# Kernel tuning notes

Hardware: AMD Instinct MI355X
Metric: run time of the kernel (lower is better)

Reference implementation:

```python
import jax, jax.numpy as jnp
import numpy as np

B, C, H, W = 16, 256, 32, 32
LN_EPS = 1e-5


def setup_inputs() -> dict:
    key = jax.random.key(0)
    ks = jax.random.split(key, 12)
    s = 1.0 / np.sqrt(C)
    x = jax.random.normal(ks[0], (B, C, H, W), dtype=jnp.float32)
    # Linear weights stored as [in, out] (torch stores [out, in]; math is x @ W_in_out + b)
    wq = jax.random.uniform(ks[1], (C, C), jnp.float32, -s, s)
    bq = jax.random.uniform(ks[2], (C,), jnp.float32, -s, s)
    wk = jax.random.uniform(ks[3], (C, C), jnp.float32, -s, s)
    bk = jax.random.uniform(ks[4], (C,), jnp.float32, -s, s)
    wv = jax.random.uniform(ks[5], (C, C), jnp.float32, -s, s)
    bv = jax.random.uniform(ks[6], (C,), jnp.float32, -s, s)
    w1 = jax.random.uniform(ks[7], (C, C), jnp.float32, -s, s)
    b1 = jax.random.uniform(ks[8], (C,), jnp.float32, -s, s)
    w2 = jax.random.uniform(ks[9], (C, C), jnp.float32, -s, s)
    b2 = jax.random.uniform(ks[10], (C,), jnp.float32, -s, s)
    gamma = jnp.ones((C,), jnp.float32)
    beta = jnp.zeros((C,), jnp.float32)
    return {"x": x, "wq": wq, "bq": bq, "wk": wk, "bk": bk, "wv": wv, "bv": bv,
            "w1": w1, "b1": b1, "w2": w2, "b2": b2, "gamma": gamma, "beta": beta}


def reference(x, wq, bq, wk, bk, wv, bv, w1, b1, w2, b2, gamma, beta):
    Bd, Cd, Hd, Wd = x.shape
    t = x.reshape(Bd, Cd, Hd * Wd).transpose(0, 2, 1)  # [B, N, C]
    q = t @ wq + bq
    k = t @ wk + bk
    v = t @ wv + bv
    # matrix[b,i,j] = q[b,i,:] . k[b,j,:]  (no 1/sqrt(d) scaling, as in source)
    m = jnp.einsum('bic,bjc->bij', q, k)
    # softmax over dim=-2 (the query axis i)
    m = jax.nn.softmax(m, axis=-2)
    # att[b,j,c] = sum_i v[b,i,c] * m[b,i,j]  (v^T @ m, then permute)
    att = jnp.einsum('bic,bij->bjc', v, m)  # [B, N, C]
    # MLP (SiLU, hidden = C), dropout p=0 -> identity; DropPath eval -> identity
    att = jax.nn.silu(att @ w1 + b1) @ w2 + b2
    # LayerNorm over channel dim
    mu = jnp.mean(att, axis=-1, keepdims=True)
    var = jnp.var(att, axis=-1, keepdims=True)
    att = (att - mu) * jax.lax.rsqrt(var + LN_EPS) * gamma + beta
    return att.transpose(0, 2, 1).reshape(Bd, Cd, Hd, Wd)
```

## Files before the change

### kernel.cpp

```cpp
#include <hip/hip_runtime.h>

#define BB 16
#define CC 256
#define NN 1024

typedef _Float16 f16;
typedef __attribute__((ext_vector_type(8))) _Float16 half8;
typedef __attribute__((ext_vector_type(4))) float f32x4;

__device__ __forceinline__ half8 ldg8(const f16* p) {
  return *reinterpret_cast<const half8*>(p);
}

__device__ __forceinline__ void gll16(const f16* g, f16* l) {
  __builtin_amdgcn_global_load_lds((const __attribute__((address_space(1))) void*)g,
                                   (__attribute__((address_space(3))) void*)l, 16, 0, 0);
}

#define VMCNT(n) asm volatile("s_waitcnt vmcnt(" #n ")" ::: "memory")
#define BAR() __builtin_amdgcn_s_barrier()

__device__ __forceinline__ void stage64k(const f16* __restrict__ g, f16* l, int wave, int lane) {
#pragma unroll
  for (int k = 0; k < 16; ++k) {
    int ob = k * 2048 + wave * 512;
    gll16(g + ob + lane * 8, l + ob);
  }
}

struct WP5 {
  const float* s[5];
  f16* d[5];
};

__global__ void __launch_bounds__(256) k_packW(WP5 p) {
  __shared__ float ws[256][17];
  int m = blockIdx.y, ct = blockIdx.x;
  const float* W = p.s[m];
  f16* wp = p.d[m];
  int tid = threadIdx.x;
  int col = tid & 15, cig = tid >> 4;
#pragma unroll
  for (int pg = 0; pg < 16; ++pg) {
    int ci = pg * 16 + cig;
    ws[ci][col] = W[(size_t)ci * 256 + ct * 16 + col];
  }
  __syncthreads();
  int lane = tid & 63, wave = tid >> 6;
  int row16 = lane & 15, quad = lane >> 4;
#pragma unroll
  for (int kk = 0; kk < 2; ++kk) {
    int kc = wave * 2 + kk;
    half8 o;
#pragma unroll
    for (int j = 0; j < 8; ++j) o[j] = (f16)ws[kc * 32 + quad * 8 + j][row16];
    *reinterpret_cast<half8*>(wp + ((size_t)ct * 8 + kc) * 512 + lane * 8) = o;
  }
}

struct QkvSmem {
  union {
    struct { f16 hi[32][264]; f16 lo[32][264]; } ts;
    f16 ex[2][16][264];
    f16 exv[256][40];
  };
};

__global__ void __launch_bounds__(256) k_qkv(const float* __restrict__ x,
    const f16* __restrict__ wqp, const f16* __restrict__ wkp, const f16* __restrict__ wvp,
    const float* __restrict__ bq, const float* __restrict__ bk, const float* __restrict__ bv,
    f16* __restrict__ qp, f16* __restrict__ kp, f16* __restrict__ vp, int b_base) {
  __shared__ QkvSmem sm;
  int z = blockIdx.z;
  const f16* WT     = (z == 0) ? wqp : (z == 1) ? wkp : wvp;
  const float* bias = (z == 0) ? bq  : (z == 1) ? bk  : bv;
  int bl = blockIdx.x, bg = b_base + bl, n0 = blockIdx.y * 32;
  int tid = threadIdx.x, wave = tid >> 6, lane = tid & 63;
  int row16 = lane & 15, quad = lane >> 4;
  int g = wave >> 1, h = wave & 1;

#pragma unroll
  for (int e = tid; e < 2048; e += 256) {
    int c = e >> 3, n4 = (e & 7) << 2;
    float4 u = *reinterpret_cast<const float4*>(x + (size_t)(bg * CC + c) * NN + n0 + n4);
    float uv[4] = {u.x, u.y, u.z, u.w};
#pragma unroll
    for (int i = 0; i < 4; ++i) {
      f16 hh = (f16)uv[i];
      sm.ts.hi[n4 + i][c] = hh;
      sm.ts.lo[n4 + i][c] = (f16)(uv[i] - (float)hh);
    }
  }
  __syncthreads();

  half8 ah[8], al[8];
#pragma unroll
  for (int kc = 0; kc < 8; ++kc) {
    ah[kc] = *reinterpret_cast<const half8*>(&sm.ts.hi[g * 16 + row16][kc * 32 + quad * 8]);
    al[kc] = *reinterpret_cast<const half8*>(&sm.ts.lo[g * 16 + row16][kc * 32 + quad * 8]);
  }
  __syncthreads();

  if (z < 2) {
    f16* outp = z ? kp : qp;
#pragma unroll
    for (int ct8 = 0; ct8 < 8; ++ct8) {
      int ct = h * 8 + ct8;
      f32x4 acc = {0.f, 0.f, 0.f, 0.f};
      const f16* bh = WT + ((size_t)ct * 8) * 512 + lane * 8;
#pragma unroll
      for (int kc = 0; kc < 8; ++kc) {
        half8 b = ldg8(bh + kc * 512);
        acc = __builtin_amdgcn_mfma_f32_16x16x32_f16(ah[kc], b, acc, 0, 0, 0);
        acc = __builtin_amdgcn_mfma_f32_16x16x32_f16(al[kc], b, acc, 0, 0, 0);
      }
      int co = ct * 16 + row16;
      float bb = bias[co];
#pragma unroll
      for (int r = 0; r < 4; ++r)
        sm.ex[g][quad * 4 + r][co] = (f16)(acc[r] + bb);
    }
    const f16* exr = &sm.ex[g][row16][0];
    size_t fb = ((size_t)bl * 64 + (n0 >> 4) + g) * 8;
#pragma unroll
    for (int k = 0; k < 4; ++k) {
      int kc = h * 4 + k;
      half8 hv = *reinterpret_cast<const half8*>(exr + kc * 32 + quad * 8);
      *reinterpret_cast<half8*>(outp + (fb + kc) * 512 + lane * 8) = hv;
    }
  } else {
#pragma unroll
    for (int ct8 = 0; ct8 < 8; ++ct8) {
      int ct = h * 8 + ct8;
      f32x4 acc = {0.f, 0.f, 0.f, 0.f};
      const f16* bh = WT + ((size_t)ct * 8) * 512 + lane * 8;
#pragma unroll
      for (int kc = 0; kc < 8; ++kc) {
        half8 b = ldg8(bh + kc * 512);
        acc = __builtin_amdgcn_mfma_f32_16x16x32_f16(ah[kc], b, acc, 0, 0, 0);
        acc = __builtin_amdgcn_mfma_f32_16x16x32_f16(al[kc], b, acc, 0, 0, 0);
      }
      int co = ct * 16 + row16;
      float bb = bias[co];
#pragma unroll
      for (int r = 0; r < 4; ++r)
        sm.exv[co][g * 16 + quad * 4 + r] = (f16)(acc[r] + bb);
    }
    __syncthreads();
    size_t vb = ((size_t)bl * 32 + blockIdx.y) * 16;
#pragma unroll
    for (int f = 0; f < 4; ++f) {
      int ct = wave * 4 + f;
      half8 o = *reinterpret_cast<const half8*>(&sm.exv[ct * 16 + row16][quad * 8]);
      *reinterpret_cast<half8*>(vp + (vb + ct) * 512 + lane * 8) = o;
    }
  }
}

struct AttnSmem {
  union {
    struct {
      f16 QB[128 * 256];
      f16 VB[128 * 256];
    } s;
    f16 ex[4][16][264];
  } u;
  f16 P[4][4][16][40];
};

__global__ void __launch_bounds__(256) k_attn_mlp(
    const f16* __restrict__ qp, const f16* __restrict__ kp, const f16* __restrict__ vp,
    const f16* __restrict__ w1p, const float* __restrict__ b1,
    const f16* __restrict__ w2p, const float* __restrict__ b2,
    const float* __restrict__ gamma, const float* __restrict__ beta,
    float* __restrict__ out, int b_base) {
  __shared__ AttnSmem sm;
  int bl = blockIdx.x, bg = b_base + bl;
  int j0 = blockIdx.y * 64;
  int tid = threadIdx.x, wave = tid >> 6, lane = tid & 63;
  int row16 = lane & 15, quad = lane >> 4;
  int jw = j0 + wave * 16;

  const f16* kbase = kp + (size_t)bl * NN * CC;
  int jt = (j0 >> 4) + wave;
  half8 kf[8];
#pragma unroll
  for (int kc = 0; kc < 8; ++kc)
    kf[kc] = ldg8(kbase + ((size_t)jt * 8 + kc) * 512 + lane * 8);

  const f16* qbase = qp + (size_t)bl * NN * CC;
  const f16* vbase = vp + (size_t)bl * CC * NN;

  stage64k(qbase, sm.u.s.QB, wave, lane);
  stage64k(vbase, sm.u.s.VB, wave, lane);
  VMCNT(16);
  BAR();

  f32x4 O[16];
#pragma unroll
  for (int ct = 0; ct < 16; ++ct) O[ct] = {0.f, 0.f, 0.f, 0.f};
  float m_run[4], l_lane[4];
#pragma unroll
  for (int r = 0; r < 4; ++r) { m_run[r] = -1e30f; l_lane[r] = 0.f; }

  for (int it = 0; it < 8; ++it) {
    f32x4 s[8];
#pragma unroll
    for (int f = 0; f < 8; ++f) s[f] = {0.f, 0.f, 0.f, 0.f};
#pragma unroll
    for (int kc = 0; kc < 8; ++kc) {
#pragma unroll
      for (int f = 0; f < 8; ++f) {
        half8 b = *reinterpret_cast<const half8*>(&sm.u.s.QB[(f * 8 + kc) * 512 + lane * 8]);
        s[f] = __builtin_amdgcn_mfma_f32_16x16x32_f16(kf[kc], b, s[f], 0, 0, 0);
      }
    }
    BAR();
    stage64k(qbase + (size_t)((it + 1) & 7) * 32768, sm.u.s.QB, wave, lane);

    float alpha[4];
#pragma unroll
    for (int r = 0; r < 4; ++r) {
      float mx = s[0][r];
#pragma unroll
      for (int f = 1; f < 8; ++f) mx = fmaxf(mx, s[f][r]);
#pragma unroll
      for (int off = 1; off < 16; off <<= 1) mx = fmaxf(mx, __shfl_xor(mx, off, 64));
      float mnew = fmaxf(m_run[r], mx);
      alpha[r] = __expf(m_run[r] - mnew);
      m_run[r] = mnew;
      float ps = 0.f;
#pragma unroll
      for (int f = 0; f < 8; ++f) {
        float pv = __expf(s[f][r] - mnew);
        ps += pv;
        sm.P[wave][f >> 1][quad * 4 + r][(f & 1) * 16 + row16] = (f16)pv;
      }
      l_lane[r] = l_lane[r] * alpha[r] + ps;
    }
#pragma unroll
    for (int ct = 0; ct < 16; ++ct)
#pragma unroll
      for (int r = 0; r < 4; ++r) O[ct][r] *= alpha[r];

    VMCNT(16);
    BAR();

#pragma unroll
    for (int c4 = 0; c4 < 4; ++c4) {
      half8 pf = *reinterpret_cast<const half8*>(&sm.P[wave][c4][row16][quad * 8]);
#pragma unroll
      for (int ct = 0; ct < 16; ++ct) {
        half8 vf = *reinterpret_cast<const half8*>(&sm.u.s.VB[(c4 * 16 + ct) * 512 + lane * 8]);
        O[ct] = __builtin_amdgcn_mfma_f32_16x16x32_f16(pf, vf, O[ct], 0, 0, 0);
      }
    }
    BAR();
    stage64k(vbase + (size_t)((it + 1) & 7) * 32768, sm.u.s.VB, wave, lane);
    VMCNT(16);
    BAR();
  }
  VMCNT(0);
  BAR();

  float inv[4];
#pragma unroll
  for (int r = 0; r < 4; ++r) {
    float l = l_lane[r];
#pragma unroll
    for (int off = 1; off < 16; off <<= 1) l += __shfl_xor(l, off, 64);
    inv[r] = 1.f / l;
  }

#pragma unroll
  for (int ct = 0; ct < 16; ++ct)
#pragma unroll
    for (int r = 0; r < 4; ++r)
      sm.u.ex[wave][quad * 4 + r][ct * 16 + row16] = (f16)(O[ct][r] * inv[r]);

  half8 af[8];
#pragma unroll
  for (int kc = 0; kc < 8; ++kc)
    af[kc] = *reinterpret_cast<const half8*>(&sm.u.ex[wave][row16][kc * 32 + quad * 8]);

#pragma unroll
  for (int ct = 0; ct < 16; ++ct) {
    f32x4 acc = {0.f, 0.f, 0.f, 0.f};
    const f16* brow = w1p + ((size_t)ct * 8) * 512 + lane * 8;
#pragma unroll
    for (int kc = 0; kc < 8; ++kc)
      acc = __builtin_amdgcn_mfma_f32_16x16x32_f16(af[kc], ldg8(brow + kc * 512), acc, 0, 0, 0);
    int co = ct * 16 + row16;
    float bb = b1[co];
#pragma unroll
    for (int r = 0; r < 4; ++r) {
      float xg = acc[r] + bb;
      float hh = xg / (1.f + __expf(-xg));
      sm.u.ex[wave][quad * 4 + r][co] = (f16)hh;
    }
  }

  half8 hf[8];
#pragma unroll
  for (int kc = 0; kc < 8; ++kc)
    hf[kc] = *reinterpret_cast<const half8*>(&sm.u.ex[wave][row16][kc * 32 + quad * 8]);

  f32x4 acc2[16];
#pragma unroll
  for (int ct = 0; ct < 16; ++ct) {
    f32x4 acc = {0.f, 0.f, 0.f, 0.f};
    const f16* brow = w2p + ((size_t)ct * 8) * 512 + lane * 8;
#pragma unroll
    for (int kc = 0; kc < 8; ++kc)
      acc = __builtin_amdgcn_mfma_f32_16x16x32_f16(hf[kc], ldg8(brow + kc * 512), acc, 0, 0, 0);
    float bb = b2[ct * 16 + row16];
#pragma unroll
    for (int r = 0; r < 4; ++r) acc[r] += bb;
    acc2[ct] = acc;
  }

  float sum[4] = {0.f, 0.f, 0.f, 0.f}, ssq[4] = {0.f, 0.f, 0.f, 0.f};
#pragma unroll
  for (int ct = 0; ct < 16; ++ct)
#pragma unroll
    for (int r = 0; r < 4; ++r) { float xv = acc2[ct][r]; sum[r] += xv; ssq[r] += xv * xv; }
  float mean[4], rstd[4];
#pragma unroll
  for (int r = 0; r < 4; ++r) {
#pragma unroll
    for (int off = 1; off < 16; off <<= 1) {
      sum[r] += __shfl_xor(sum[r], off, 64);
      ssq[r] += __shfl_xor(ssq[r], off, 64);
    }
    mean[r] = sum[r] * (1.f / 256.f);
    float var = ssq[r] * (1.f / 256.f) - mean[r] * mean[r];
    rstd[r] = rsqrtf(var + 1e-5f);
  }

#pragma unroll
  for (int ct = 0; ct < 16; ++ct) {
    int col = ct * 16 + row16;
    float g = gamma[col], be = beta[col];
    f32x4 v;
#pragma unroll
    for (int r = 0; r < 4; ++r) v[r] = (acc2[ct][r] - mean[r]) * rstd[r] * g + be;
    *reinterpret_cast<f32x4*>(out + (size_t)(bg * CC + col) * NN + jw + quad * 4) = v;
  }
}

extern "C" void kernel_launch(void* const* d_in, const int* in_sizes, int n_in,
                              void* d_out, int out_size, void* d_ws, size_t ws_size,
                              hipStream_t stream) {
  (void)in_sizes; (void)n_in; (void)out_size;
  const float* x     = (const float*)d_in[0];
  const float* wq    = (const float*)d_in[1];
  const float* bq    = (const float*)d_in[2];
  const float* wk    = (const float*)d_in[3];
  const float* bk    = (const float*)d_in[4];
  const float* wv    = (const float*)d_in[5];
  const float* bv    = (const float*)d_in[6];
  const float* w1    = (const float*)d_in[7];
  const float* b1    = (const float*)d_in[8];
  const float* w2    = (const float*)d_in[9];
  const float* b2    = (const float*)d_in[10];
  const float* gamma = (const float*)d_in[11];
  const float* beta  = (const float*)d_in[12];
  float* out = (float*)d_out;

  const size_t WE = 65536;
  const size_t SB = (size_t)NN * CC;
  f16* base = (f16*)d_ws;
  f16* wqp = base + 0 * WE;
  f16* wkp = base + 1 * WE;
  f16* wvp = base + 2 * WE;
  f16* w1p = base + 3 * WE;
  f16* w2p = base + 4 * WE;

  size_t wbytes = 5 * WE * sizeof(f16);
  size_t perb   = 3 * SB * sizeof(f16);
  int nb = (ws_size > wbytes) ? (int)((ws_size - wbytes) / perb) : 1;
  if (nb < 1) nb = 1;
  if (nb > BB) nb = BB;

  f16* qb  = base + 5 * WE;
  f16* kb  = qb + (size_t)nb * SB;
  f16* vTb = kb + (size_t)nb * SB;

  WP5 p;
  p.s[0] = wq; p.s[1] = wk; p.s[2] = wv; p.s[3] = w1; p.s[4] = w2;
  p.d[0] = wqp; p.d[1] = wkp; p.d[2] = wvp; p.d[3] = w1p; p.d[4] = w2p;
  k_packW<<<dim3(16, 5), 256, 0, stream>>>(p);

  for (int b0 = 0; b0 < BB; b0 += nb) {
    int cb = (b0 + nb <= BB) ? nb : (BB - b0);
    k_qkv<<<dim3(cb, 32, 3), 256, 0, stream>>>(x, wqp, wkp, wvp, bq, bk, bv, qb, kb, vTb, b0);
    k_attn_mlp<<<dim3(cb, 16), 256, 0, stream>>>(qb, kb, vTb, w1p, b1, w2p, b2,
                                                 gamma, beta, out, b0);
  }
}
```

Baseline: 203.0 us.

## Fuse Q, K, V projections into one block and interleave independent MFMA chains

The QKV kernel no longer launches three grid slices along z. Each block now converts its x tile to hi/lo halves once and computes Q, K and V in sequence, removing the repeated x load and conversion. The inner loop keeps four output tiles in flight, with separate hi and lo accumulators, so MFMA dependency chains are independent and weight loads can overlap. The trade-off is a third as many blocks, longer per-block work, more registers and extra barriers, which can reduce occupancy and parallelism.

```diff
diff --git a/kernel.cpp b/kernel.cpp
--- a/kernel.cpp
+++ b/kernel.cpp
@@ -71,9 +71,6 @@
     const float* __restrict__ bq, const float* __restrict__ bk, const float* __restrict__ bv,
     f16* __restrict__ qp, f16* __restrict__ kp, f16* __restrict__ vp, int b_base) {
   __shared__ QkvSmem sm;
-  int z = blockIdx.z;
-  const f16* WT     = (z == 0) ? wqp : (z == 1) ? wkp : wvp;
-  const float* bias = (z == 0) ? bq  : (z == 1) ? bk  : bv;
   int bl = blockIdx.x, bg = b_base + bl, n0 = blockIdx.y * 32;
   int tid = threadIdx.x, wave = tid >> 6, lane = tid & 63;
   int row16 = lane & 15, quad = lane >> 4;
@@ -101,24 +98,38 @@
   }
   __syncthreads();
 
-  if (z < 2) {
-    f16* outp = z ? kp : qp;
-#pragma unroll
-    for (int ct8 = 0; ct8 < 8; ++ct8) {
-      int ct = h * 8 + ct8;
-      f32x4 acc = {0.f, 0.f, 0.f, 0.f};
-      const f16* bh = WT + ((size_t)ct * 8) * 512 + lane * 8;
+  const f16* WTs[2]    = {wqp, wkp};
+  const float* biases[2] = {bq, bk};
+  f16* outs[2]         = {qp, kp};
+#pragma unroll
+  for (int z = 0; z < 2; ++z) {
+    const f16* WT = WTs[z];
+    const float* bias = biases[z];
+    f16* outp = outs[z];
+#pragma unroll
+    for (int cp = 0; cp < 2; ++cp) {
+      f32x4 acch[4], accl[4];
+#pragma unroll
+      for (int u = 0; u < 4; ++u) { acch[u] = {0.f,0.f,0.f,0.f}; accl[u] = {0.f,0.f,0.f,0.f}; }
 #pragma unroll
       for (int kc = 0; kc < 8; ++kc) {
-        half8 b = ldg8(bh + kc * 512);
-        acc = __builtin_amdgcn_mfma_f32_16x16x32_f16(ah[kc], b, acc, 0, 0, 0);
-        acc = __builtin_amdgcn_mfma_f32_16x16x32_f16(al[kc], b, acc, 0, 0, 0);
-      }
-      int co = ct * 16 + row16;
-      float bb = bias[co];
-#pragma unroll
-      for (int r = 0; r < 4; ++r)
-        sm.ex[g][quad * 4 + r][co] = (f16)(acc[r] + bb);
+#pragma unroll
+        for (int u = 0; u < 4; ++u) {
+          int ct = h * 8 + cp * 4 + u;
+          half8 b = ldg8(WT + ((size_t)ct * 8 + kc) * 512 + lane * 8);
+          acch[u] = __builtin_amdgcn_mfma_f32_16x16x32_f16(ah[kc], b, acch[u], 0, 0, 0);
+          accl[u] = __builtin_amdgcn_mfma_f32_16x16x32_f16(al[kc], b, accl[u], 0, 0, 0);
+        }
+      }
+#pragma unroll
+      for (int u = 0; u < 4; ++u) {
+        int ct = h * 8 + cp * 4 + u;
+        int co = ct * 16 + row16;
+        float bb = bias[co];
+#pragma unroll
+        for (int r = 0; r < 4; ++r)
+          sm.ex[g][quad * 4 + r][co] = (f16)(acch[u][r] + accl[u][r] + bb);
+      }
     }
     const f16* exr = &sm.ex[g][row16][0];
     size_t fb = ((size_t)bl * 64 + (n0 >> 4) + g) * 8;
@@ -128,32 +139,41 @@
       half8 hv = *reinterpret_cast<const half8*>(exr + kc * 32 + quad * 8);
       *reinterpret_cast<half8*>(outp + (fb + kc) * 512 + lane * 8) = hv;
     }
-  } else {
-#pragma unroll
-    for (int ct8 = 0; ct8 < 8; ++ct8) {
-      int ct = h * 8 + ct8;
-      f32x4 acc = {0.f, 0.f, 0.f, 0.f};
-      const f16* bh = WT + ((size_t)ct * 8) * 512 + lane * 8;
-#pragma unroll
-      for (int kc = 0; kc < 8; ++kc) {
-        half8 b = ldg8(bh + kc * 512);
-        acc = __builtin_amdgcn_mfma_f32_16x16x32_f16(ah[kc], b, acc, 0, 0, 0);
-        acc = __builtin_amdgcn_mfma_f32_16x16x32_f16(al[kc], b, acc, 0, 0, 0);
-      }
+  }
+  __syncthreads();
+
+#pragma unroll
+  for (int cp = 0; cp < 2; ++cp) {
+    f32x4 acch[4], accl[4];
+#pragma unroll
+    for (int u = 0; u < 4; ++u) { acch[u] = {0.f,0.f,0.f,0.f}; accl[u] = {0.f,0.f,0.f,0.f}; }
+#pragma unroll
+    for (int kc = 0; kc < 8; ++kc) {
+#pragma unroll
+      for (int u = 0; u < 4; ++u) {
+        int ct = h * 8 + cp * 4 + u;
+        half8 b = ldg8(wvp + ((size_t)ct * 8 + kc) * 512 + lane * 8);
+        acch[u] = __builtin_amdgcn_mfma_f32_16x16x32_f16(ah[kc], b, acch[u], 0, 0, 0);
+        accl[u] = __builtin_amdgcn_mfma_f32_16x16x32_f16(al[kc], b, accl[u], 0, 0, 0);
+      }
+    }
+#pragma unroll
+    for (int u = 0; u < 4; ++u) {
+      int ct = h * 8 + cp * 4 + u;
       int co = ct * 16 + row16;
-      float bb = bias[co];
+      float bb = bv[co];
 #pragma unroll
       for (int r = 0; r < 4; ++r)
-        sm.exv[co][g * 16 + quad * 4 + r] = (f16)(acc[r] + bb);
-    }
-    __syncthreads();
-    size_t vb = ((size_t)bl * 32 + blockIdx.y) * 16;
-#pragma unroll
-    for (int f = 0; f < 4; ++f) {
-      int ct = wave * 4 + f;
-      half8 o = *reinterpret_cast<const half8*>(&sm.exv[ct * 16 + row16][quad * 8]);
-      *reinterpret_cast<half8*>(vp + (vb + ct) * 512 + lane * 8) = o;
-    }
+        sm.exv[co][g * 16 + quad * 4 + r] = (f16)(acch[u][r] + accl[u][r] + bb);
+    }
+  }
+  __syncthreads();
+  size_t vb = ((size_t)bl * 32 + blockIdx.y) * 16;
+#pragma unroll
+  for (int f = 0; f < 4; ++f) {
+    int ct = wave * 4 + f;
+    half8 o = *reinterpret_cast<const half8*>(&sm.exv[ct * 16 + row16][quad * 8]);
+    *reinterpret_cast<half8*>(vp + (vb + ct) * 512 + lane * 8) = o;
   }
 }
 
@@ -393,7 +413,7 @@
 
   for (int b0 = 0; b0 < BB; b0 += nb) {
     int cb = (b0 + nb <= BB) ? nb : (BB - b0);
-    k_qkv<<<dim3(cb, 32, 3), 256, 0, stream>>>(x, wqp, wkp, wvp, bq, bk, bv, qb, kb, vTb, b0);
+    k_qkv<<<dim3(cb, 32), 256, 0, stream>>>(x, wqp, wkp, wvp, bq, bk, bv, qb, kb, vTb, b0);
     k_attn_mlp<<<dim3(cb, 16), 256, 0, stream>>>(qb, kb, vTb, w1p, b1, w2p, b2,
                                                  gamma, beta, out, b0);
   }
```

Result: no change. 199.6 us (-1.7%).
